# Kernel tuning notes

Hardware: AMD Instinct MI355X
Metric: run time of the kernel (lower is better)

The kernel has to match this reference:

```python
import jax, jax.numpy as jnp
import numpy as np
from jax import lax

FPS_NUM, K = 2048, 32


def fps_subsample(x, n):
    # x: [B, N, 3] -> [B, n, 3]; farthest point sampling, deterministic start at index 0
    B, N, _ = x.shape
    d0 = jnp.sum((x - x[:, :1]) ** 2, axis=-1)  # [B, N] dist to point 0

    def step(dists, _):
        nxt = jnp.argmax(dists, axis=1)                       # [B]
        p = x[jnp.arange(B), nxt]                             # [B, 3]
        dists = jnp.minimum(dists, jnp.sum((x - p[:, None]) ** 2, axis=-1))
        return dists, nxt

    _, idxs = lax.scan(step, d0, None, length=n - 1)          # [n-1, B]
    idxs = jnp.concatenate([jnp.zeros((1, B), jnp.int32), idxs.astype(jnp.int32)], axis=0).T  # [B, n]
    return x[jnp.arange(B)[:, None], idxs]                    # [B, n, 3]


def knn_idx(x, k):
    # x: [B, C, N] -> [B, N, k] indices of k nearest neighbors in feature space
    xx = jnp.sum(x * x, axis=1)                               # [B, N]
    inner = jnp.einsum('bcn,bcm->bnm', x, x)
    neg_dist = 2.0 * inner - xx[:, :, None] - xx[:, None, :]  # -||xi-xj||^2
    return lax.top_k(neg_dist, k)[1]


def get_graph_feature(x, k):
    # DGCNN edge features: x [B, C, N] -> [B, 2C, N, k]
    B, C, N = x.shape
    idx = knn_idx(x, k)                                       # [B, N, k]
    xt = jnp.transpose(x, (0, 2, 1))                          # [B, N, C]
    nbr = xt[jnp.arange(B)[:, None, None], idx]               # [B, N, k, C]
    ctr = jnp.broadcast_to(xt[:, :, None], nbr.shape)
    feat = jnp.concatenate([nbr - ctr, ctr], axis=-1)         # [B, N, k, 2C]
    return jnp.transpose(feat, (0, 3, 1, 2))


def attention(xq, xk, pos, Wq, bq, Wk, bk, Wv, bv, Wp, bp):
    # positional attention over k neighbors: xq/xk [B, Cin, N, k], pos [B, 3, N] -> [B, dim, N]
    q = jnp.einsum('bcnk,dc->bdnk', xq, Wq) + bq[:, None, None]
    kk = jnp.einsum('bcnk,dc->bdnk', xk, Wk) + bk[:, None, None]
    v = jnp.einsum('bcnk,dc->bdnk', xk, Wv) + bv[:, None, None]
    p = jnp.einsum('bcn,dc->bdn', pos, Wp) + bp[:, None]      # [B, dim, N]
    dim = Wq.shape[0]
    logits = jnp.einsum('bdnk,bdnk->bnk', q, kk) / jnp.sqrt(jnp.float32(dim))
    attn = jax.nn.softmax(logits, axis=-1)                    # [B, N, k]
    return jnp.einsum('bnk,bdnk->bdn', attn, v + p[:, :, :, None])


def _layer_params(key, cin, dim):
    ks = jax.random.split(key, 4)
    s = 1.0 / np.sqrt(cin)
    return (jax.random.normal(ks[0], (dim, cin), jnp.float32) * s,
            jnp.zeros((dim,), jnp.float32),
            jax.random.normal(ks[1], (dim, cin), jnp.float32) * s,
            jnp.zeros((dim,), jnp.float32),
            jax.random.normal(ks[2], (dim, cin), jnp.float32) * s,
            jnp.zeros((dim,), jnp.float32),
            jax.random.normal(ks[3], (dim, 3), jnp.float32) * (1.0 / np.sqrt(3.0)),
            jnp.zeros((dim,), jnp.float32))


def setup_inputs() -> dict:
    key = jax.random.key(0)
    kx, k1, k2, k3 = jax.random.split(key, 4)
    x = jax.random.normal(kx, (8, 16384, 3), jnp.float32)
    out = {'x': x}
    for name, kk_, cin, dim in (('t1', k1, 6, 64), ('t2', k2, 128, 64), ('t3', k3, 128, 128)):
        Wq, bq, Wk, bk, Wv, bv, Wp, bp = _layer_params(kk_, cin, dim)
        out.update({f'{name}_Wq': Wq, f'{name}_bq': bq, f'{name}_Wk': Wk, f'{name}_bk': bk,
                    f'{name}_Wv': Wv, f'{name}_bv': bv, f'{name}_Wp': Wp, f'{name}_bp': bp})
    return out


def reference(x, t1_Wq, t1_bq, t1_Wk, t1_bk, t1_Wv, t1_bv, t1_Wp, t1_bp,
              t2_Wq, t2_bq, t2_Wk, t2_bk, t2_Wv, t2_bv, t2_Wp, t2_bp,
              t3_Wq, t3_bq, t3_Wk, t3_bk, t3_Wv, t3_bv, t3_Wp, t3_bp):
    partial = jnp.transpose(fps_subsample(x, FPS_NUM), (0, 2, 1))       # [B, 3, n]
    g = get_graph_feature(partial, K)                                    # [B, 6, n, k]
    x1 = attention(g, g, partial, t1_Wq, t1_bq, t1_Wk, t1_bk, t1_Wv, t1_bv, t1_Wp, t1_bp)  # [B, 64, n]
    g = get_graph_feature(x1, K)                                         # [B, 128, n, k]
    x2 = attention(g, g, partial, t2_Wq, t2_bq, t2_Wk, t2_bk, t2_Wv, t2_bv, t2_Wp, t2_bp)  # [B, 64, n]
    g = get_graph_feature(x2, K)                                         # [B, 128, n, k]
    x3 = attention(g, g, partial, t3_Wq, t3_bq, t3_Wk, t3_bk, t3_Wv, t3_bv, t3_Wp, t3_bp)  # [B, 128, n]
    feats = jnp.concatenate([x1, x2, x3], axis=1)                        # [B, 256, n]
    return jnp.concatenate([jnp.max(feats, axis=-1), jnp.mean(feats, axis=-1)], axis=1)    # [B, 512]
```

## Files before the change

kernel.cpp:

```cpp
#include <hip/hip_runtime.h>
#include <math.h>

#define NB 8
#define NIN 16384
#define NP 2048
#define KNN 32
#define TOTPTS (NB * NP)

#define NEG_INF (-__builtin_inff())
#define POS_INF (__builtin_inff())

__device__ __forceinline__ float2 pk_add(float2 a, float2 b) {
  float2 d;
  asm("v_pk_add_f32 %0, %1, %2" : "=v"(d) : "v"(a), "v"(b));
  return d;
}
__device__ __forceinline__ float2 pk_mul(float2 a, float2 b) {
  float2 d;
  asm("v_pk_mul_f32 %0, %1, %2" : "=v"(d) : "v"(a), "v"(b));
  return d;
}

#define DPP_F(old, v, C, RM) \
  __int_as_float(__builtin_amdgcn_update_dpp(__float_as_int(old), __float_as_int(v), C, RM, 0xf, false))
#define DPP_I(old, v, C, RM) \
  __builtin_amdgcn_update_dpp(old, v, C, RM, 0xf, false)

__device__ __forceinline__ float wave_max_f(float v) {
  v = fmaxf(v, DPP_F(NEG_INF, v, 0x111, 0xf));
  v = fmaxf(v, DPP_F(NEG_INF, v, 0x112, 0xf));
  v = fmaxf(v, DPP_F(NEG_INF, v, 0x114, 0xf));
  v = fmaxf(v, DPP_F(NEG_INF, v, 0x118, 0xf));
  v = fmaxf(v, DPP_F(NEG_INF, v, 0x142, 0xa));
  v = fmaxf(v, DPP_F(NEG_INF, v, 0x143, 0xc));
  return v;
}
__device__ __forceinline__ int wave_min_i(int v) {
  v = min(v, DPP_I(0x7fffffff, v, 0x111, 0xf));
  v = min(v, DPP_I(0x7fffffff, v, 0x112, 0xf));
  v = min(v, DPP_I(0x7fffffff, v, 0x114, 0xf));
  v = min(v, DPP_I(0x7fffffff, v, 0x118, 0xf));
  v = min(v, DPP_I(0x7fffffff, v, 0x142, 0xa));
  v = min(v, DPP_I(0x7fffffff, v, 0x143, 0xc));
  return v;
}

__device__ __forceinline__ float readlane63f(float v) {
  return __int_as_float(__builtin_amdgcn_readlane(__float_as_int(v), 63));
}

__global__ __launch_bounds__(1024) void fps_kernel(const float* __restrict__ x,
                                                   float* __restrict__ partial) {
  const int b = blockIdx.x;
  const int t = threadIdx.x;
  const int w = t >> 6, l = t & 63;
  const float* xb = x + (size_t)b * NIN * 3;
  float* pb = partial + (size_t)b * NP * 3;
  __shared__ unsigned long long skey[NP][2];
  __shared__ float4 swave[2][16];
  for (int i = t; i < NP; i += 1024) { skey[i][0] = 0ull; skey[i][1] = 0ull; }

  float2 px[8], py[8], pz[8], dd[8];
#pragma unroll
  for (int j = 0; j < 8; ++j) {
    const int i0 = (2 * j) * 1024 + t, i1 = (2 * j + 1) * 1024 + t;
    px[j] = make_float2(xb[3 * i0], xb[3 * i1]);
    py[j] = make_float2(xb[3 * i0 + 1], xb[3 * i1 + 1]);
    pz[j] = make_float2(xb[3 * i0 + 2], xb[3 * i1 + 2]);
  }
  const float qx0 = xb[0], qy0 = xb[1], qz0 = xb[2];
  if (t == 0) { pb[0] = qx0; pb[1] = qy0; pb[2] = qz0; }

  float bv = NEG_INF;
  int bi = 0;
  {
    const float2 nx2 = make_float2(-qx0, -qx0);
    const float2 ny2 = make_float2(-qy0, -qy0);
    const float2 nz2 = make_float2(-qz0, -qz0);
#pragma unroll
    for (int j = 0; j < 8; ++j) {
      float2 dx = pk_add(px[j], nx2), dy = pk_add(py[j], ny2), dz = pk_add(pz[j], nz2);
      float2 nd = pk_add(pk_add(pk_mul(dx, dx), pk_mul(dy, dy)), pk_mul(dz, dz));
      dd[j] = nd;
      if (nd.x > bv) { bv = nd.x; bi = (2 * j) * 1024 + t; }
      if (nd.y > bv) { bv = nd.y; bi = (2 * j + 1) * 1024 + t; }
    }
  }

  {
    const float wm = wave_max_f(bv);
    const float smaxw = readlane63f(wm);
    const int sel = (bv == smaxw) ? bi : 0x7fffffff;
    const int wiw = __builtin_amdgcn_readlane(wave_min_i(sel), 63);
    const float ax = xb[3 * wiw], ay = xb[3 * wiw + 1], az = xb[3 * wiw + 2];
    if (l == 63) {
      const unsigned long long key =
          ((unsigned long long)__float_as_uint(smaxw) << 32) | (unsigned int)(~wiw);
      atomicMax(&skey[1][w & 1], key);
    }
    if (l == 0) swave[1][w] = make_float4(ax, ay, az, 0.f);
  }
  __syncthreads();

  for (int it = 1; it < NP; ++it) {
    const unsigned long long k0 = skey[it][0], k1 = skey[it][1];
    const unsigned long long gk = (k0 > k1) ? k0 : k1;
    const int gbi = (int)(~(unsigned int)gk);
    const int wstar = (gbi >> 6) & 15;
    const float4 qc = swave[it & 1][wstar];
    const float nqx = qc.x, nqy = qc.y, nqz = qc.z;
    if (t == 0) { pb[3 * it] = nqx; pb[3 * it + 1] = nqy; pb[3 * it + 2] = nqz; }

    const float2 nx2 = make_float2(-nqx, -nqx);
    const float2 ny2 = make_float2(-nqy, -nqy);
    const float2 nz2 = make_float2(-nqz, -nqz);
    bv = NEG_INF;
    bi = 0;
#pragma unroll
    for (int j = 0; j < 8; ++j) {
      float2 dx = pk_add(px[j], nx2), dy = pk_add(py[j], ny2), dz = pk_add(pz[j], nz2);
      float2 nd = pk_add(pk_add(pk_mul(dx, dx), pk_mul(dy, dy)), pk_mul(dz, dz));
      const float a0 = fminf(dd[j].x, nd.x);
      dd[j].x = a0;
      if (a0 > bv) { bv = a0; bi = (2 * j) * 1024 + t; }
      const float a1 = fminf(dd[j].y, nd.y);
      dd[j].y = a1;
      if (a1 > bv) { bv = a1; bi = (2 * j + 1) * 1024 + t; }
    }

    if (it + 1 < NP) {
      const float wm = wave_max_f(bv);
      const float smaxw = readlane63f(wm);
      const int sel = (bv == smaxw) ? bi : 0x7fffffff;
      const int wiw = __builtin_amdgcn_readlane(wave_min_i(sel), 63);
      const float ax = xb[3 * wiw], ay = xb[3 * wiw + 1], az = xb[3 * wiw + 2];
      if (l == 63) {
        const unsigned long long key =
            ((unsigned long long)__float_as_uint(smaxw) << 32) | (unsigned int)(~wiw);
        atomicMax(&skey[it + 1][w & 1], key);
      }
      if (l == 0) swave[(it + 1) & 1][w] = make_float4(ax, ay, az, 0.f);
    }
    __syncthreads();
  }
}

__global__ void xx_kernel(const float* __restrict__ F, float* __restrict__ xxg, int C) {
  int i = blockIdx.x * 256 + threadIdx.x;
  if (i >= TOTPTS) return;
  const float* f = F + (size_t)i * C;
  float s = 0.f;
  for (int c = 0; c < C; ++c) s = __fadd_rn(s, __fmul_rn(f[c], f[c]));
  xxg[i] = s;
}

__global__ __launch_bounds__(1024) void knn3_kernel(const float* __restrict__ F,
                                                    int* __restrict__ idxg) {
  const int b = blockIdx.z;
  const int t = threadIdx.x;
  const int w = t >> 6, lane = t & 63;
  __shared__ float spx[NP], spy[NP], spz[NP], sxx[NP];
  const float* Fb = F + (size_t)b * NP * 3;
  for (int i = t; i < NP; i += 1024) {
    const float a0 = Fb[3 * i], a1 = Fb[3 * i + 1], a2 = Fb[3 * i + 2];
    spx[i] = a0; spy[i] = a1; spz[i] = a2;
    float s = __fadd_rn(0.f, __fmul_rn(a0, a0));
    s = __fadd_rn(s, __fmul_rn(a1, a1));
    s = __fadd_rn(s, __fmul_rn(a2, a2));
    sxx[i] = s;
  }
  __syncthreads();
  const int row = blockIdx.x * 16 + w;
  const float a0 = spx[row], a1 = spy[row], a2 = spz[row];
  const float xn = sxx[row];
  float v[32];
#pragma unroll
  for (int s = 0; s < 32; ++s) {
    const int m = s * 64 + lane;
    float acc = fmaf(a0, spx[m], 0.f);
    acc = fmaf(a1, spy[m], acc);
    acc = fmaf(a2, spz[m], acc);
    v[s] = __fsub_rn(__fsub_rn(2.0f * acc, xn), sxx[m]);
  }
  int* out = idxg + ((size_t)b * NP + row) * KNN;
  for (int tt = 0; tt < KNN; ++tt) {
    float bv = v[0];
    int bs = 0;
#pragma unroll
    for (int s = 1; s < 32; ++s) {
      if (v[s] > bv) { bv = v[s]; bs = s; }
    }
    int bi = bs * 64 + lane;
    const float vmax = readlane63f(wave_max_f(bv));
    const int sel = (bv == vmax) ? bi : 0x7fffffff;
    const int wbi = __builtin_amdgcn_readlane(wave_min_i(sel), 63);
    if (lane == 0) out[tt] = wbi;
    const bool own = (lane == (wbi & 63));
    const int cs = wbi >> 6;
#pragma unroll
    for (int s = 0; s < 32; ++s)
      if (own && s == cs) v[s] = NEG_INF;
  }
}

template <int C>
__global__ __launch_bounds__(256) void dist_gemm(const float* __restrict__ F,
                                                 const float* __restrict__ xxg,
                                                 float* __restrict__ D, int bofs) {
  __shared__ float As[64][C + 1];
  __shared__ float Bs[64][C + 1];
  const int b = bofs + blockIdx.z;
  float* Ds = D + (size_t)blockIdx.z * NP * NP;
  const int tid = threadIdx.x;
  const int n0 = blockIdx.y * 64, m0 = blockIdx.x * 64;
  const float* Fb = F + (size_t)b * NP * C;
  const float* xxb = xxg + b * NP;
  for (int t = tid; t < 64 * C; t += 256) {
    int r = t / C, c = t - r * C;
    As[r][c] = Fb[(size_t)(n0 + r) * C + c];
    Bs[r][c] = Fb[(size_t)(m0 + r) * C + c];
  }
  __syncthreads();
  const int tx = tid & 15, ty = tid >> 4;
  float acc[4][4] = {};
  for (int c = 0; c < C; ++c) {
    float a[4], bb[4];
#pragma unroll
    for (int i = 0; i < 4; ++i) a[i] = As[ty * 4 + i][c];
#pragma unroll
    for (int j = 0; j < 4; ++j) bb[j] = Bs[tx * 4 + j][c];
#pragma unroll
    for (int i = 0; i < 4; ++i)
#pragma unroll
      for (int j = 0; j < 4; ++j) acc[i][j] = fmaf(a[i], bb[j], acc[i][j]);
  }
#pragma unroll
  for (int i = 0; i < 4; ++i) {
    int n = n0 + ty * 4 + i;
    float xn = xxb[n];
    float4 o;
    o.x = __fsub_rn(__fsub_rn(2.0f * acc[i][0], xn), xxb[m0 + tx * 4 + 0]);
    o.y = __fsub_rn(__fsub_rn(2.0f * acc[i][1], xn), xxb[m0 + tx * 4 + 1]);
    o.z = __fsub_rn(__fsub_rn(2.0f * acc[i][2], xn), xxb[m0 + tx * 4 + 2]);
    o.w = __fsub_rn(__fsub_rn(2.0f * acc[i][3], xn), xxb[m0 + tx * 4 + 3]);
    *(float4*)&Ds[(size_t)n * NP + m0 + tx * 4] = o;
  }
}

__global__ __launch_bounds__(256) void select_kernel(const float* __restrict__ D,
                                                     int* __restrict__ idxg, int bofs) {
  const int lane = threadIdx.x & 63;
  const int b = bofs + blockIdx.z;
  const int row = blockIdx.x * 4 + (threadIdx.x >> 6);
  const float* Drow = D + (size_t)blockIdx.z * NP * NP + (size_t)row * NP;
  float v[32];
#pragma unroll
  for (int s = 0; s < 32; ++s) v[s] = Drow[s * 64 + lane];
  int* out = idxg + ((size_t)b * NP + row) * KNN;
  for (int t = 0; t < KNN; ++t) {
    float bv = v[0];
    int bs = 0;
#pragma unroll
    for (int s = 1; s < 32; ++s) {
      if (v[s] > bv) { bv = v[s]; bs = s; }
    }
    int bi = bs * 64 + lane;
    const float vmax = readlane63f(wave_max_f(bv));
    const int sel = (bv == vmax) ? bi : 0x7fffffff;
    const int wbi = __builtin_amdgcn_readlane(wave_min_i(sel), 63);
    if (lane == 0) out[t] = wbi;
    const bool own = (lane == (wbi & 63));
    const int cs = wbi >> 6;
#pragma unroll
    for (int s = 0; s < 32; ++s)
      if (own && s == cs) v[s] = NEG_INF;
  }
}

template <int C, int DIM>
__global__ __launch_bounds__(256) void proj_kernel(
    const float* __restrict__ F, const float* __restrict__ pos,
    const float* __restrict__ Wq, const float* __restrict__ bq,
    const float* __restrict__ Wk, const float* __restrict__ bk,
    const float* __restrict__ Wv, const float* __restrict__ bv,
    const float* __restrict__ Wp, const float* __restrict__ bp,
    float* __restrict__ Uq, float* __restrict__ Uk, float* __restrict__ Uv,
    float* __restrict__ Uqc, float* __restrict__ Ukc, float* __restrict__ W6) {
  constexpr int PTS = 16;
  constexpr int GROUPS = 256 / DIM;
  constexpr int PPT = PTS / GROUPS;
  __shared__ float xs[PTS][C];
  __shared__ float ps[PTS][3];
  const int tid = threadIdx.x;
  const int base = blockIdx.x * PTS;
  for (int t = tid; t < PTS * C; t += 256) {
    int r = t / C;
    xs[r][t - r * C] = F[(size_t)(base + r) * C + (t - r * C)];
  }
  for (int t = tid; t < PTS * 3; t += 256) {
    int r = t / 3;
    ps[r][t - r * 3] = pos[(size_t)(base + r) * 3 + (t - r * 3)];
  }
  __syncthreads();
  const int g = tid / DIM;
  const int d = tid - g * DIM;
  float uq[PPT], uqd[PPT], uk[PPT], ukd[PPT], uv[PPT], uvd[PPT];
#pragma unroll
  for (int p = 0; p < PPT; ++p) { uq[p] = uqd[p] = uk[p] = ukd[p] = uv[p] = uvd[p] = 0.f; }
  const float* wqr = Wq + (size_t)d * (2 * C);
  const float* wkr = Wk + (size_t)d * (2 * C);
  const float* wvr = Wv + (size_t)d * (2 * C);
  for (int c = 0; c < C; ++c) {
    const float wq1 = wqr[c], wqd_ = wqr[C + c] - wq1;
    const float wk1 = wkr[c], wkd_ = wkr[C + c] - wk1;
    const float wv1 = wvr[c], wvd_ = wvr[C + c] - wv1;
#pragma unroll
    for (int p = 0; p < PPT; ++p) {
      const float xc = xs[g + p * GROUPS][c];
      uq[p] = fmaf(wq1, xc, uq[p]);
      uqd[p] = fmaf(wqd_, xc, uqd[p]);
      uk[p] = fmaf(wk1, xc, uk[p]);
      ukd[p] = fmaf(wkd_, xc, ukd[p]);
      uv[p] = fmaf(wv1, xc, uv[p]);
      uvd[p] = fmaf(wvd_, xc, uvd[p]);
    }
  }
  const float bqd = bq[d], bkd = bk[d], bvd = bv[d];
  const float wp0 = Wp[d * 3], wp1 = Wp[d * 3 + 1], wp2 = Wp[d * 3 + 2], bpd = bp[d];
#pragma unroll
  for (int p = 0; p < PPT; ++p) {
    const int lp = g + p * GROUPS;
    const size_t o = (size_t)(base + lp) * DIM + d;
    const float pd = wp0 * ps[lp][0] + wp1 * ps[lp][1] + wp2 * ps[lp][2] + bpd;
    Uq[o] = uq[p];
    Uqc[o] = uqd[p] + bqd;
    Uk[o] = uk[p];
    Ukc[o] = ukd[p] + bkd;
    Uv[o] = uv[p];
    W6[o] = uvd[p] + bvd + pd;
  }
}

template <int DIM>
__global__ void prep_kernel(const float* __restrict__ Wq, const float* __restrict__ bq,
                            const float* __restrict__ Wk, const float* __restrict__ bk,
                            const float* __restrict__ Wv, const float* __restrict__ bv,
                            float* __restrict__ Wcat, float* __restrict__ bcat) {
  const int o = blockIdx.x * 256 + threadIdx.x;
  constexpr int ND = 6 * DIM;
  if (o >= ND) return;
  const int blk = o / DIM, d = o % DIM;
  bcat[o] = (blk == 1) ? bq[d] : (blk == 3) ? bk[d] : (blk == 5) ? bv[d] : 0.f;
  const float* W = (blk < 2) ? Wq : (blk < 4) ? Wk : Wv;
  for (int c = 0; c < 64; ++c) {
    const float w1 = W[(size_t)d * 128 + c];
    const float w2 = W[(size_t)d * 128 + 64 + c];
    Wcat[(size_t)c * ND + o] = (blk & 1) ? (w2 - w1) : w1;
  }
}

template <int DIM>
__global__ __launch_bounds__(256) void gemm_proj(
    const float* __restrict__ F, const float* __restrict__ Wcat,
    const float* __restrict__ bcat, const float* __restrict__ pos,
    const float* __restrict__ Wp, const float* __restrict__ bp,
    float* __restrict__ Uq, float* __restrict__ Uqc, float* __restrict__ Uk,
    float* __restrict__ Ukc, float* __restrict__ Uv, float* __restrict__ W6) {
  constexpr int ND = 6 * DIM;
  __shared__ float As[64][65];
  __shared__ float Bs[64][65];
  const int tid = threadIdx.x;
  const int r0blk = blockIdx.x * 64;
  const int n0 = blockIdx.y * 64;
  {
    const int r0 = tid >> 4, c4 = (tid & 15) * 4;
    for (int r = r0; r < 64; r += 16) {
      float4 a = *(const float4*)&F[(size_t)(r0blk + r) * 64 + c4];
      As[r][c4] = a.x; As[r][c4 + 1] = a.y; As[r][c4 + 2] = a.z; As[r][c4 + 3] = a.w;
      float4 bb = *(const float4*)&Wcat[(size_t)r * ND + n0 + c4];
      Bs[r][c4] = bb.x; Bs[r][c4 + 1] = bb.y; Bs[r][c4 + 2] = bb.z; Bs[r][c4 + 3] = bb.w;
    }
  }
  __syncthreads();
  const int tx = tid & 15, ty = tid >> 4;
  float acc[4][4] = {};
#pragma unroll 4
  for (int c = 0; c < 64; ++c) {
    float a[4], bb[4];
#pragma unroll
    for (int i = 0; i < 4; ++i) a[i] = As[ty * 4 + i][c];
#pragma unroll
    for (int j = 0; j < 4; ++j) bb[j] = Bs[c][tx * 4 + j];
#pragma unroll
    for (int i = 0; i < 4; ++i)
#pragma unroll
      for (int j = 0; j < 4; ++j) acc[i][j] = fmaf(a[i], bb[j], acc[i][j]);
  }
  const int obuf = n0 / DIM;
  const int oloc = n0 - obuf * DIM;
  float* outp = (obuf == 0) ? Uq : (obuf == 1) ? Uqc : (obuf == 2) ? Uk
              : (obuf == 3) ? Ukc : (obuf == 4) ? Uv : W6;
  const float b0 = bcat[n0 + tx * 4], b1 = bcat[n0 + tx * 4 + 1];
  const float b2 = bcat[n0 + tx * 4 + 2], b3 = bcat[n0 + tx * 4 + 3];
  float wpx[4], wpy[4], wpz[4], bpv[4];
  if (obuf == 5) {
#pragma unroll
    for (int j = 0; j < 4; ++j) {
      const int oc = oloc + tx * 4 + j;
      wpx[j] = Wp[oc * 3]; wpy[j] = Wp[oc * 3 + 1]; wpz[j] = Wp[oc * 3 + 2];
      bpv[j] = bp[oc];
    }
  }
#pragma unroll
  for (int i = 0; i < 4; ++i) {
    const int p = r0blk + ty * 4 + i;
    float4 r = make_float4(acc[i][0] + b0, acc[i][1] + b1, acc[i][2] + b2, acc[i][3] + b3);
    if (obuf == 5) {
      const float q0 = pos[(size_t)p * 3], q1 = pos[(size_t)p * 3 + 1], q2 = pos[(size_t)p * 3 + 2];
      r.x += wpx[0] * q0 + wpy[0] * q1 + wpz[0] * q2 + bpv[0];
      r.y += wpx[1] * q0 + wpy[1] * q1 + wpz[1] * q2 + bpv[1];
      r.z += wpx[2] * q0 + wpy[2] * q1 + wpz[2] * q2 + bpv[2];
      r.w += wpx[3] * q0 + wpy[3] * q1 + wpz[3] * q2 + bpv[3];
    }
    *(float4*)&outp[(size_t)p * DIM + oloc + tx * 4] = r;
  }
}

template <int DIM>
__global__ __launch_bounds__(256) void attn_kernel(
    const float* __restrict__ Uq, const float* __restrict__ Uk, const float* __restrict__ Uv,
    const float* __restrict__ Uqc, const float* __restrict__ Ukc, const float* __restrict__ W6g,
    const int* __restrict__ idxg, float* __restrict__ outF) {
  const int w = threadIdx.x >> 6, lane = threadIdx.x & 63;
  const int pt = blockIdx.x * 4 + w;
  const int b = pt >> 11;
  __shared__ int sidx[4][KNN];
  __shared__ float sqc[4][DIM], skc[4][DIM], sw6[4][DIM];
  __shared__ float sattn[4][KNN];
  const size_t rowo = (size_t)pt * DIM;
  if (lane < KNN) sidx[w][lane] = idxg[(size_t)pt * KNN + lane];
  for (int d = lane; d < DIM; d += 64) {
    sqc[w][d] = Uqc[rowo + d];
    skc[w][d] = Ukc[rowo + d];
    sw6[w][d] = W6g[rowo + d];
  }
  __syncthreads();
  {
    const int kk = lane & 31;
    const int h = lane >> 5;
    const int ik = sidx[w][kk];
    const float* qr = Uq + (size_t)(b * NP + ik) * DIM;
    const float* kr = Uk + (size_t)(b * NP + ik) * DIM;
    float lg = 0.f;
    const int d0 = h * (DIM / 2), d1 = d0 + DIM / 2;
    for (int d = d0; d < d1; d += 4) {
      float4 qa = *(const float4*)(qr + d);
      float4 ka = *(const float4*)(kr + d);
      float4 qc = *(const float4*)(&sqc[w][d]);
      float4 kc = *(const float4*)(&skc[w][d]);
      lg += (qa.x + qc.x) * (ka.x + kc.x);
      lg += (qa.y + qc.y) * (ka.y + kc.y);
      lg += (qa.z + qc.z) * (ka.z + kc.z);
      lg += (qa.w + qc.w) * (ka.w + kc.w);
    }
    lg += __shfl_xor(lg, 32);
    lg *= (DIM == 64) ? 0.125f : 0.08838834764831845f;
    float m = lg;
#pragma unroll
    for (int off = 16; off; off >>= 1) m = fmaxf(m, __shfl_xor(m, off));
    float e = expf(lg - m);
    float s = e;
#pragma unroll
    for (int off = 16; off; off >>= 1) s += __shfl_xor(s, off);
    if (lane < KNN) sattn[w][lane] = e / s;
  }
  __syncthreads();
  float acc[DIM / 64];
#pragma unroll
  for (int q = 0; q < DIM / 64; ++q) acc[q] = 0.f;
  for (int k = 0; k < KNN; ++k) {
    const int ik = sidx[w][k];
    const float a = sattn[w][k];
    const float* vr = Uv + (size_t)(b * NP + ik) * DIM;
#pragma unroll
    for (int q = 0; q < DIM / 64; ++q) {
      const int d = q * 64 + lane;
      acc[q] = fmaf(a, vr[d] + sw6[w][d], acc[q]);
    }
  }
#pragma unroll
  for (int q = 0; q < DIM / 64; ++q) outF[rowo + q * 64 + lane] = acc[q];
}

#define PCHUNKS 16
__global__ __launch_bounds__(256) void pool1_kernel(const float* __restrict__ x1,
                                                    const float* __restrict__ x2,
                                                    const float* __restrict__ x3,
                                                    float* __restrict__ pmax,
                                                    float* __restrict__ psum) {
  const int b = blockIdx.x, ch = blockIdx.y, c = threadIdx.x;
  const float* src;
  int dim, cl;
  if (c < 64) {
    src = x1 + (size_t)b * NP * 64; dim = 64; cl = c;
  } else if (c < 128) {
    src = x2 + (size_t)b * NP * 64; dim = 64; cl = c - 64;
  } else {
    src = x3 + (size_t)b * NP * 128; dim = 128; cl = c - 128;
  }
  const int n0 = ch * (NP / PCHUNKS), n1 = n0 + NP / PCHUNKS;
  float mx = NEG_INF, sm = 0.f;
#pragma unroll 8
  for (int n = n0; n < n1; ++n) {
    float v = src[(size_t)n * dim + cl];
    mx = fmaxf(mx, v);
    sm += v;
  }
  const size_t o = ((size_t)b * PCHUNKS + ch) * 256 + c;
  pmax[o] = mx;
  psum[o] = sm;
}

__global__ __launch_bounds__(256) void pool2_kernel(const float* __restrict__ pmax,
                                                    const float* __restrict__ psum,
                                                    float* __restrict__ out) {
  const int b = blockIdx.x, c = threadIdx.x;
  float mx = NEG_INF, sm = 0.f;
#pragma unroll
  for (int ch = 0; ch < PCHUNKS; ++ch) {
    const size_t o = ((size_t)b * PCHUNKS + ch) * 256 + c;
    mx = fmaxf(mx, pmax[o]);
    sm += psum[o];
  }
  out[b * 512 + c] = mx;
  out[b * 512 + 256 + c] = sm * (1.0f / 2048.0f);
}

extern "C" void kernel_launch(void* const* d_in, const int* in_sizes, int n_in,
                              void* d_out, int out_size, void* d_ws, size_t ws_size,
                              hipStream_t stream) {
  const float* x = (const float*)d_in[0];
  const float* W[24];
  for (int i = 0; i < 24; ++i) W[i] = (const float*)d_in[1 + i];

  float* ws = (float*)d_ws;
  size_t off = 0;
  float* partial = ws + off; off += (size_t)NB * NP * 3;
  float* xxbuf = ws + off;   off += TOTPTS;
  int* idxb = (int*)(ws + off); off += (size_t)TOTPTS * KNN;
  float* x1 = ws + off; off += (size_t)TOTPTS * 64;
  float* x2 = ws + off; off += (size_t)TOTPTS * 64;
  float* x3 = ws + off; off += (size_t)TOTPTS * 128;
  float* Uq = ws + off;  off += (size_t)TOTPTS * 128;
  float* Uk = ws + off;  off += (size_t)TOTPTS * 128;
  float* Uv = ws + off;  off += (size_t)TOTPTS * 128;
  float* Uqc = ws + off; off += (size_t)TOTPTS * 128;
  float* Ukc = ws + off; off += (size_t)TOTPTS * 128;
  float* W6 = ws + off;  off += (size_t)TOTPTS * 128;
  float* Wcat = ws + off; off += (size_t)64 * 768;
  float* bcat = ws + off; off += 768;
  float* pmax = ws + off; off += (size_t)NB * PCHUNKS * 256;
  float* psum = ws + off; off += (size_t)NB * PCHUNKS * 256;
  if (ws_size < off * sizeof(float)) return;

  float* Dbig = ws + off;
  const size_t need_big = (off + (size_t)NB * NP * NP) * sizeof(float);
  const bool bigws = (ws_size >= need_big);
  float* D = bigws ? Dbig : Uq;
  const int NZ = bigws ? NB : 1;

  fps_kernel<<<NB, 1024, 0, stream>>>(x, partial);

  knn3_kernel<<<dim3(NP / 16, 1, NB), 1024, 0, stream>>>(partial, idxb);
  proj_kernel<3, 64><<<TOTPTS / 16, 256, 0, stream>>>(
      partial, partial, W[0], W[1], W[2], W[3], W[4], W[5], W[6], W[7],
      Uq, Uk, Uv, Uqc, Ukc, W6);
  attn_kernel<64><<<TOTPTS / 4, 256, 0, stream>>>(Uq, Uk, Uv, Uqc, Ukc, W6, idxb, x1);

  xx_kernel<<<TOTPTS / 256, 256, 0, stream>>>(x1, xxbuf, 64);
  for (int b = 0; b < NB; b += NZ) {
    dist_gemm<64><<<dim3(32, 32, NZ), 256, 0, stream>>>(x1, xxbuf, D, b);
    select_kernel<<<dim3(NP / 4, 1, NZ), 256, 0, stream>>>(D, idxb, b);
  }
  prep_kernel<64><<<2, 256, 0, stream>>>(W[8], W[9], W[10], W[11], W[12], W[13], Wcat, bcat);
  gemm_proj<64><<<dim3(TOTPTS / 64, 6), 256, 0, stream>>>(
      x1, Wcat, bcat, partial, W[14], W[15], Uq, Uqc, Uk, Ukc, Uv, W6);
  attn_kernel<64><<<TOTPTS / 4, 256, 0, stream>>>(Uq, Uk, Uv, Uqc, Ukc, W6, idxb, x2);

  xx_kernel<<<TOTPTS / 256, 256, 0, stream>>>(x2, xxbuf, 64);
  for (int b = 0; b < NB; b += NZ) {
    dist_gemm<64><<<dim3(32, 32, NZ), 256, 0, stream>>>(x2, xxbuf, D, b);
    select_kernel<<<dim3(NP / 4, 1, NZ), 256, 0, stream>>>(D, idxb, b);
  }
  prep_kernel<128><<<3, 256, 0, stream>>>(W[16], W[17], W[18], W[19], W[20], W[21], Wcat, bcat);
  gemm_proj<128><<<dim3(TOTPTS / 64, 12), 256, 0, stream>>>(
      x2, Wcat, bcat, partial, W[22], W[23], Uq, Uqc, Uk, Ukc, Uv, W6);
  attn_kernel<128><<<TOTPTS / 4, 256, 0, stream>>>(Uq, Uk, Uv, Uqc, Ukc, W6, idxb, x3);

  pool1_kernel<<<dim3(NB, PCHUNKS), 256, 0, stream>>>(x1, x2, x3, pmax, psum);
  pool2_kernel<<<NB, 256, 0, stream>>>(pmax, psum, (float*)d_out);
}
```

Baseline: 4.460 ms.

## Fuse 64-dim kNN distance GEMM, norms and top-k selection into one kernel

Replaces the xx_kernel, the dist_gemm that writes a full 2048x2048 distance matrix per batch, and the separate select_kernel with one knn64_kernel. Each wave keeps its query row in registers, streams 256-point tiles of features through shared memory, computes distances and norms on the fly, and runs the wave-level top-32 selection directly on register values. This removes the large global-memory round trip for the distance matrix and several launches. The cost is lower arithmetic reuse: it is a per-row dot product rather than a register-blocked GEMM, each block recomputes the tile norms, and the 64-float query array raises register pressure.

New measurement: 4.895 ms. 1.1x slower.

```diff
diff --git a/kernel.cpp b/kernel.cpp
--- a/kernel.cpp
+++ b/kernel.cpp
@@ -143,15 +143,6 @@
     }
     __syncthreads();
   }
-}
-
-__global__ void xx_kernel(const float* __restrict__ F, float* __restrict__ xxg, int C) {
-  int i = blockIdx.x * 256 + threadIdx.x;
-  if (i >= TOTPTS) return;
-  const float* f = F + (size_t)i * C;
-  float s = 0.f;
-  for (int c = 0; c < C; ++c) s = __fadd_rn(s, __fmul_rn(f[c], f[c]));
-  xxg[i] = s;
 }
 
 __global__ __launch_bounds__(1024) void knn3_kernel(const float* __restrict__ F,
@@ -203,61 +194,56 @@
   }
 }
 
-template <int C>
-__global__ __launch_bounds__(256) void dist_gemm(const float* __restrict__ F,
-                                                 const float* __restrict__ xxg,
-                                                 float* __restrict__ D, int bofs) {
-  __shared__ float As[64][C + 1];
-  __shared__ float Bs[64][C + 1];
-  const int b = bofs + blockIdx.z;
-  float* Ds = D + (size_t)blockIdx.z * NP * NP;
-  const int tid = threadIdx.x;
-  const int n0 = blockIdx.y * 64, m0 = blockIdx.x * 64;
-  const float* Fb = F + (size_t)b * NP * C;
-  const float* xxb = xxg + b * NP;
-  for (int t = tid; t < 64 * C; t += 256) {
-    int r = t / C, c = t - r * C;
-    As[r][c] = Fb[(size_t)(n0 + r) * C + c];
-    Bs[r][c] = Fb[(size_t)(m0 + r) * C + c];
-  }
-  __syncthreads();
-  const int tx = tid & 15, ty = tid >> 4;
-  float acc[4][4] = {};
-  for (int c = 0; c < C; ++c) {
-    float a[4], bb[4];
-#pragma unroll
-    for (int i = 0; i < 4; ++i) a[i] = As[ty * 4 + i][c];
-#pragma unroll
-    for (int j = 0; j < 4; ++j) bb[j] = Bs[tx * 4 + j][c];
-#pragma unroll
-    for (int i = 0; i < 4; ++i)
-#pragma unroll
-      for (int j = 0; j < 4; ++j) acc[i][j] = fmaf(a[i], bb[j], acc[i][j]);
-  }
-#pragma unroll
-  for (int i = 0; i < 4; ++i) {
-    int n = n0 + ty * 4 + i;
-    float xn = xxb[n];
-    float4 o;
-    o.x = __fsub_rn(__fsub_rn(2.0f * acc[i][0], xn), xxb[m0 + tx * 4 + 0]);
-    o.y = __fsub_rn(__fsub_rn(2.0f * acc[i][1], xn), xxb[m0 + tx * 4 + 1]);
-    o.z = __fsub_rn(__fsub_rn(2.0f * acc[i][2], xn), xxb[m0 + tx * 4 + 2]);
-    o.w = __fsub_rn(__fsub_rn(2.0f * acc[i][3], xn), xxb[m0 + tx * 4 + 3]);
-    *(float4*)&Ds[(size_t)n * NP + m0 + tx * 4] = o;
-  }
-}
-
-__global__ __launch_bounds__(256) void select_kernel(const float* __restrict__ D,
-                                                     int* __restrict__ idxg, int bofs) {
-  const int lane = threadIdx.x & 63;
-  const int b = bofs + blockIdx.z;
-  const int row = blockIdx.x * 4 + (threadIdx.x >> 6);
-  const float* Drow = D + (size_t)blockIdx.z * NP * NP + (size_t)row * NP;
+__global__ __launch_bounds__(512) void knn64_kernel(const float* __restrict__ F,
+                                                    int* __restrict__ idxg) {
+  const int b = blockIdx.z;
+  const int t = threadIdx.x;
+  const int w = t >> 6, lane = t & 63;
+  const int row = blockIdx.x * 8 + w;
+  __shared__ float tile[256][65];
+  __shared__ float sxx[256];
+  __shared__ float srow[8][65];
+  const float* Fb = F + (size_t)b * NP * 64;
+  for (int i = t; i < 8 * 64; i += 512) {
+    const int r = i >> 6, c = i & 63;
+    srow[r][c] = Fb[(size_t)(blockIdx.x * 8 + r) * 64 + c];
+  }
+  __syncthreads();
+  float a[64];
+#pragma unroll
+  for (int c = 0; c < 64; ++c) a[c] = srow[w][c];
+  float xn = 0.f;
+#pragma unroll
+  for (int c = 0; c < 64; ++c) xn = __fadd_rn(xn, __fmul_rn(a[c], a[c]));
+
   float v[32];
-#pragma unroll
-  for (int s = 0; s < 32; ++s) v[s] = Drow[s * 64 + lane];
+  for (int tt = 0; tt < 8; ++tt) {
+    __syncthreads();
+    for (int i = t; i < 256 * 16; i += 512) {
+      const int r = i >> 4, c4 = (i & 15) * 4;
+      float4 q = *(const float4*)&Fb[(size_t)(tt * 256 + r) * 64 + c4];
+      tile[r][c4] = q.x; tile[r][c4 + 1] = q.y;
+      tile[r][c4 + 2] = q.z; tile[r][c4 + 3] = q.w;
+    }
+    __syncthreads();
+    for (int i = t; i < 256; i += 512) {
+      float s = 0.f;
+      for (int c = 0; c < 64; ++c) s = __fadd_rn(s, __fmul_rn(tile[i][c], tile[i][c]));
+      sxx[i] = s;
+    }
+    __syncthreads();
+#pragma unroll
+    for (int u = 0; u < 4; ++u) {
+      const int ml = u * 64 + lane;
+      float acc = 0.f;
+#pragma unroll
+      for (int c = 0; c < 64; ++c) acc = fmaf(a[c], tile[ml][c], acc);
+      v[tt * 4 + u] = __fsub_rn(__fsub_rn(2.0f * acc, xn), sxx[ml]);
+    }
+  }
+
   int* out = idxg + ((size_t)b * NP + row) * KNN;
-  for (int t = 0; t < KNN; ++t) {
+  for (int ttk = 0; ttk < KNN; ++ttk) {
     float bv = v[0];
     int bs = 0;
 #pragma unroll
@@ -268,7 +254,7 @@
     const float vmax = readlane63f(wave_max_f(bv));
     const int sel = (bv == vmax) ? bi : 0x7fffffff;
     const int wbi = __builtin_amdgcn_readlane(wave_min_i(sel), 63);
-    if (lane == 0) out[t] = wbi;
+    if (lane == 0) out[ttk] = wbi;
     const bool own = (lane == (wbi & 63));
     const int cs = wbi >> 6;
 #pragma unroll
@@ -546,7 +532,6 @@
   float* ws = (float*)d_ws;
   size_t off = 0;
   float* partial = ws + off; off += (size_t)NB * NP * 3;
-  float* xxbuf = ws + off;   off += TOTPTS;
   int* idxb = (int*)(ws + off); off += (size_t)TOTPTS * KNN;
   float* x1 = ws + off; off += (size_t)TOTPTS * 64;
   float* x2 = ws + off; off += (size_t)TOTPTS * 64;
@@ -563,12 +548,6 @@
   float* psum = ws + off; off += (size_t)NB * PCHUNKS * 256;
   if (ws_size < off * sizeof(float)) return;
 
-  float* Dbig = ws + off;
-  const size_t need_big = (off + (size_t)NB * NP * NP) * sizeof(float);
-  const bool bigws = (ws_size >= need_big);
-  float* D = bigws ? Dbig : Uq;
-  const int NZ = bigws ? NB : 1;
-
   fps_kernel<<<NB, 1024, 0, stream>>>(x, partial);
 
   knn3_kernel<<<dim3(NP / 16, 1, NB), 1024, 0, stream>>>(partial, idxb);
@@ -577,21 +556,13 @@
       Uq, Uk, Uv, Uqc, Ukc, W6);
   attn_kernel<64><<<TOTPTS / 4, 256, 0, stream>>>(Uq, Uk, Uv, Uqc, Ukc, W6, idxb, x1);
 
-  xx_kernel<<<TOTPTS / 256, 256, 0, stream>>>(x1, xxbuf, 64);
-  for (int b = 0; b < NB; b += NZ) {
-    dist_gemm<64><<<dim3(32, 32, NZ), 256, 0, stream>>>(x1, xxbuf, D, b);
-    select_kernel<<<dim3(NP / 4, 1, NZ), 256, 0, stream>>>(D, idxb, b);
-  }
+  knn64_kernel<<<dim3(NP / 8, 1, NB), 512, 0, stream>>>(x1, idxb);
   prep_kernel<64><<<2, 256, 0, stream>>>(W[8], W[9], W[10], W[11], W[12], W[13], Wcat, bcat);
   gemm_proj<64><<<dim3(TOTPTS / 64, 6), 256, 0, stream>>>(
       x1, Wcat, bcat, partial, W[14], W[15], Uq, Uqc, Uk, Ukc, Uv, W6);
   attn_kernel<64><<<TOTPTS / 4, 256, 0, stream>>>(Uq, Uk, Uv, Uqc, Ukc, W6, idxb, x2);
 
-  xx_kernel<<<TOTPTS / 256, 256, 0, stream>>>(x2, xxbuf, 64);
-  for (int b = 0; b < NB; b += NZ) {
-    dist_gemm<64><<<dim3(32, 32, NZ), 256, 0, stream>>>(x2, xxbuf, D, b);
-    select_kernel<<<dim3(NP / 4, 1, NZ), 256, 0, stream>>>(D, idxb, b);
-  }
+  knn64_kernel<<<dim3(NP / 8, 1, NB), 512, 0, stream>>>(x2, idxb);
   prep_kernel<128><<<3, 256, 0, stream>>>(W[16], W[17], W[18], W[19], W[20], W[21], Wcat, bcat);
   gemm_proj<128><<<dim3(TOTPTS / 64, 12), 256, 0, stream>>>(
       x2, Wcat, bcat, partial, W[22], W[23], Uq, Uqc, Uk, Ukc, Uv, W6);
```
